# Kernel optimization log

Hardware: AMD Instinct MI355X
Metric: run time of the kernel (lower is better)

The kernel has to match this reference:

```python
import jax, jax.numpy as jnp
import numpy as np

N = 100000   # nodes
E = 1600000  # edges
F = 128      # node features
H = 64       # hidden_dim
G = 64       # graphs in batch


def setup_inputs() -> dict:
    key = jax.random.key(0)
    ks = jax.random.split(key, 12)
    x = jax.random.normal(ks[0], (N, F), jnp.float32)
    edge_index = jax.random.randint(ks[1], (2, E), 0, N, dtype=jnp.int64)
    batch = jnp.sort(jax.random.randint(ks[2], (N,), 0, G, dtype=jnp.int64))
    s = 0.05
    W1 = jax.random.normal(ks[3], (F, H), jnp.float32) * s
    b1 = jnp.zeros((H,), jnp.float32)
    W2 = jax.random.normal(ks[4], (H, H), jnp.float32) * s
    b2 = jnp.zeros((H,), jnp.float32)
    Wa = jax.random.normal(ks[5], (H, 1), jnp.float32) * s
    ba = jnp.zeros((1,), jnp.float32)
    Wc = jax.random.normal(ks[6], (H, 1), jnp.float32) * s
    bc = jnp.zeros((1,), jnp.float32)
    return {"x": x, "edge_index": edge_index, "batch": batch,
            "W1": W1, "b1": b1, "W2": W2, "b2": b2,
            "Wa": Wa, "ba": ba, "Wc": Wc, "bc": bc}


def _gcn_norm(edge_index, n):
    # Add self-loops, compute symmetric normalization deg^-1/2[src]*deg^-1/2[dst]
    loop = jnp.arange(n, dtype=edge_index.dtype)
    src = jnp.concatenate([edge_index[0], loop])
    dst = jnp.concatenate([edge_index[1], loop])
    deg = jax.ops.segment_sum(jnp.ones_like(src, jnp.float32), dst, num_segments=n)
    dinv = jnp.where(deg > 0, deg ** -0.5, 0.0)
    norm = dinv[src] * dinv[dst]  # [E+N]
    return src, dst, norm


def _gcn_conv(x, W, b, src, dst, norm, n):
    h = x @ W                         # [n, H] dense transform first (PyG order)
    msg = h[src] * norm[:, None]      # gather + normalize [E+n, H]
    agg = jax.ops.segment_sum(msg, dst, num_segments=n)  # scatter-add
    return agg + b


def reference(x, edge_index, batch, W1, b1, W2, b2, Wa, ba, Wc, bc):
    n = x.shape[0]
    src, dst, norm = _gcn_norm(edge_index, n)
    h = jax.nn.relu(_gcn_conv(x, W1, b1, src, dst, norm, n))
    # dropout p=0.1 is identity in eval mode
    h = jax.nn.relu(_gcn_conv(h, W2, b2, src, dst, norm, n))
    action_logits = (h @ Wa + ba)[:, 0]  # [N]
    counts = jax.ops.segment_sum(jnp.ones((n,), jnp.float32), batch, num_segments=G)
    pooled = jax.ops.segment_sum(h, batch, num_segments=G) / jnp.maximum(counts, 1.0)[:, None]
    value = pooled @ Wc + bc  # [G, 1]
    return action_logits, value
```

## Files before the change

### kernel.cpp

```cpp
#include <hip/hip_runtime.h>
#include <hip/hip_fp16.h>
#include <math.h>

#define FEAT 128
#define HID  64
#define BSH  7
#define BNODES (1 << BSH)
#define PB   256
#define SRCM ((1u << 25) - 1)


__global__ void part_hist_k(const int* __restrict__ dst, int* __restrict__ table,
                            int e, int nb) {
    __shared__ int lcnt[1024];
    for (int i = threadIdx.x; i < nb; i += 256) lcnt[i] = 0;
    __syncthreads();
    int eb = (e + PB - 1) / PB;
    int lo = blockIdx.x * eb, hi = min(lo + eb, e);
    for (int i = lo + threadIdx.x; i < hi; i += 256)
        atomicAdd(&lcnt[dst[i] >> BSH], 1);
    __syncthreads();
    for (int k = threadIdx.x; k < nb; k += 256)
        table[k * PB + blockIdx.x] = lcnt[k];
}

__global__ void scan1_k(int* __restrict__ data, int* __restrict__ aux, int L) {
    __shared__ int s[1024];
    int gid = blockIdx.x * 1024 + threadIdx.x;
    int v = (gid < L) ? data[gid] : 0;
    s[threadIdx.x] = v;
    __syncthreads();
    for (int off = 1; off < 1024; off <<= 1) {
        int t = (threadIdx.x >= off) ? s[threadIdx.x - off] : 0;
        __syncthreads();
        s[threadIdx.x] += t;
        __syncthreads();
    }
    if (gid < L) data[gid] = s[threadIdx.x] - v;
    if (threadIdx.x == 1023) aux[blockIdx.x] = s[1023];
}

__global__ void scan2_k(int* aux, int naux) {
    __shared__ int s[1024];
    int v = (threadIdx.x < naux) ? aux[threadIdx.x] : 0;
    s[threadIdx.x] = v;
    __syncthreads();
    for (int off = 1; off < 1024; off <<= 1) {
        int t = (threadIdx.x >= off) ? s[threadIdx.x - off] : 0;
        __syncthreads();
        s[threadIdx.x] += t;
        __syncthreads();
    }
    if (threadIdx.x < naux) aux[threadIdx.x] = s[threadIdx.x] - v;
}

__global__ void part_scatter_k(const int* __restrict__ src, const int* __restrict__ dst,
                               const int* __restrict__ table, const int* __restrict__ aux,
                               unsigned* __restrict__ packed, int e, int nb) {
    __shared__ int loff[1024];
    for (int k = threadIdx.x; k < nb; k += 256) {
        int idx = k * PB + blockIdx.x;
        loff[k] = table[idx] + aux[idx >> 10];
    }
    __syncthreads();
    int eb = (e + PB - 1) / PB;
    int lo = blockIdx.x * eb, hi = min(lo + eb, e);
    for (int i = lo + threadIdx.x; i < hi; i += 256) {
        int d = dst[i];
        int p = atomicAdd(&loff[d >> BSH], 1);
        packed[p] = ((unsigned)(d & (BNODES - 1)) << 25) | (unsigned)src[i];
    }
}


__global__ void bucket_sort_k(const unsigned* __restrict__ packed,
                              const int* __restrict__ table, const int* __restrict__ aux,
                              int* __restrict__ col, int* __restrict__ rowptr,
                              float* __restrict__ dinv, int n, int e, int nb) {
    __shared__ int cnt[BNODES];
    __shared__ int s[BNODES];
    __shared__ int cur[BNODES];
    const int k = blockIdx.x;
    const int t = threadIdx.x;
    if (t < BNODES) cnt[t] = 0;
    __syncthreads();
    int i0 = k * PB;
    int i1 = (k + 1) * PB;
    const int bs = table[i0] + aux[i0 >> 10];
    const int be = (k + 1 < nb) ? (table[i1] + aux[i1 >> 10]) : e;
    for (int i = bs + t; i < be; i += 256)
        atomicAdd(&cnt[packed[i] >> 25], 1);
    __syncthreads();
    if (t < BNODES) s[t] = cnt[t];
    __syncthreads();
    for (int off = 1; off < BNODES; off <<= 1) {
        int v = (t < BNODES && t >= off) ? s[t - off] : 0;
        __syncthreads();
        if (t < BNODES) s[t] += v;
        __syncthreads();
    }
    if (t < BNODES) {
        int base = bs + s[t] - cnt[t];
        cur[t] = base;
        int node = (k << BSH) + t;
        if (node < n) {
            rowptr[node] = base;
            dinv[node] = 1.0f / sqrtf(1.0f + (float)cnt[t]);
            if (node == n - 1) rowptr[n] = base + cnt[t];
        }
    }
    __syncthreads();
    for (int i = bs + t; i < be; i += 256) {
        unsigned u = packed[i];
        int p = atomicAdd(&cur[u >> 25], 1);
        col[p] = (int)(u & SRCM);
    }
}


template<int K, bool IN16>
__global__ __launch_bounds__(256, (K == 128) ? 3 : 4)
void gemm_tile_k(const void* __restrict__ Xv, const float* __restrict__ W,
                 const float* __restrict__ dinv, __half* __restrict__ out, int n) {
    __shared__ float sX[64][K + 4];
    __shared__ float sW[64][64];
    const int row0 = blockIdx.x * 64;
    const int t  = threadIdx.x;
    const int tx = t & 15;
    const int ty = t >> 4;
    constexpr int KSH = (K == 128) ? 7 : 6;

    if constexpr (!IN16) {
        const float* xb = (const float*)Xv + (size_t)row0 * K;
#pragma unroll
        for (int it = 0; it < K / 16; ++it) {
            int fl = it * 1024 + t * 4;
            int r  = fl >> KSH;
            int k  = fl & (K - 1);
            float4 v = make_float4(0.f, 0.f, 0.f, 0.f);
            if (row0 + r < n) v = *(const float4*)(xb + fl);
            *(float4*)&sX[r][k] = v;
        }
    } else {
        const __half* xb = (const __half*)Xv + (size_t)row0 * K;
#pragma unroll
        for (int it = 0; it < K / 32; ++it) {
            int fl = it * 2048 + t * 8;
            int r  = fl >> KSH;
            int k  = fl & (K - 1);
            float4 raw = make_float4(0.f, 0.f, 0.f, 0.f);
            if (row0 + r < n) raw = *(const float4*)(xb + fl);
            const __half2* hp = (const __half2*)&raw;
#pragma unroll
            for (int j = 0; j < 4; ++j) {
                float2 f = __half22float2(hp[j]);
                sX[r][k + 2 * j]     = f.x;
                sX[r][k + 2 * j + 1] = f.y;
            }
        }
    }

    float acc[4][4] = {};
#pragma unroll
    for (int ph = 0; ph < K / 64; ++ph) {
        __syncthreads();
#pragma unroll
        for (int it = 0; it < 4; ++it) {
            int fl = it * 1024 + t * 4;
            *(float4*)&sW[fl >> 6][fl & 63] = *(const float4*)(W + ph * 64 * HID + fl);
        }
        __syncthreads();

#pragma unroll 8
        for (int k = 0; k < 64; k += 4) {
            float4 a[4], b[4];
#pragma unroll
            for (int i = 0; i < 4; i++) a[i] = *(float4*)&sX[ty * 4 + i][ph * 64 + k];
#pragma unroll
            for (int j = 0; j < 4; j++) b[j] = *(float4*)&sW[k + j][tx * 4];
#pragma unroll
            for (int i = 0; i < 4; i++) {
                acc[i][0] = fmaf(a[i].x, b[0].x, acc[i][0]);
                acc[i][1] = fmaf(a[i].x, b[0].y, acc[i][1]);
                acc[i][2] = fmaf(a[i].x, b[0].z, acc[i][2]);
                acc[i][3] = fmaf(a[i].x, b[0].w, acc[i][3]);
                acc[i][0] = fmaf(a[i].y, b[1].x, acc[i][0]);
                acc[i][1] = fmaf(a[i].y, b[1].y, acc[i][1]);
                acc[i][2] = fmaf(a[i].y, b[1].z, acc[i][2]);
                acc[i][3] = fmaf(a[i].y, b[1].w, acc[i][3]);
                acc[i][0] = fmaf(a[i].z, b[2].x, acc[i][0]);
                acc[i][1] = fmaf(a[i].z, b[2].y, acc[i][1]);
                acc[i][2] = fmaf(a[i].z, b[2].z, acc[i][2]);
                acc[i][3] = fmaf(a[i].z, b[2].w, acc[i][3]);
                acc[i][0] = fmaf(a[i].w, b[3].x, acc[i][0]);
                acc[i][1] = fmaf(a[i].w, b[3].y, acc[i][1]);
                acc[i][2] = fmaf(a[i].w, b[3].z, acc[i][2]);
                acc[i][3] = fmaf(a[i].w, b[3].w, acc[i][3]);
            }
        }
    }

#pragma unroll
    for (int i = 0; i < 4; i++) {
        int gr = row0 + ty * 4 + i;
        if (gr < n) {
            float sc = dinv[gr];
            union { __half2 h[2]; unsigned long long u; } pk;
            pk.h[0] = __floats2half2_rn(acc[i][0] * sc, acc[i][1] * sc);
            pk.h[1] = __floats2half2_rn(acc[i][2] * sc, acc[i][3] * sc);
            *(unsigned long long*)(out + (size_t)gr * HID + tx * 4) = pk.u;
        }
    }
}


template<bool LOGITS>
__global__ void gather_k(const __half* __restrict__ tS, const int* __restrict__ rowptr,
                         const int* __restrict__ col, const float* __restrict__ dinv,
                         const float* __restrict__ b, __half* __restrict__ out,
                         const float* __restrict__ Wa, const float* __restrict__ ba,
                         float* __restrict__ logits, int n) {
    int node = (int)((blockIdx.x * (size_t)blockDim.x + threadIdx.x) >> 5);
    int lane = threadIdx.x & 31;
    if (node >= n) return;
    int beg = rowptr[node], end = rowptr[node + 1];
    const __half2* tl = (const __half2*)tS + lane;
    float2 acc = __half22float2(tl[node * 32]);
    int e = beg;
    for (; e + 16 <= end; e += 16) {
        int s[16];
        __half2 v[16];
#pragma unroll
        for (int j = 0; j < 16; j++) s[j] = col[e + j];
#pragma unroll
        for (int j = 0; j < 16; j++) v[j] = tl[s[j] * 32];
        float2 t0 = make_float2(0.f, 0.f), t1 = make_float2(0.f, 0.f);
#pragma unroll
        for (int j = 0; j < 8; j++) {
            float2 f = __half22float2(v[j]);
            t0.x += f.x; t0.y += f.y;
        }
#pragma unroll
        for (int j = 8; j < 16; j++) {
            float2 f = __half22float2(v[j]);
            t1.x += f.x; t1.y += f.y;
        }
        acc.x += t0.x + t1.x;
        acc.y += t0.y + t1.y;
    }
    for (; e + 4 <= end; e += 4) {
        __half2 v0 = tl[col[e] * 32];
        __half2 v1 = tl[col[e + 1] * 32];
        __half2 v2 = tl[col[e + 2] * 32];
        __half2 v3 = tl[col[e + 3] * 32];
        float2 f0 = __half22float2(v0), f1 = __half22float2(v1);
        float2 f2 = __half22float2(v2), f3 = __half22float2(v3);
        acc.x += (f0.x + f1.x) + (f2.x + f3.x);
        acc.y += (f0.y + f1.y) + (f2.y + f3.y);
    }
    for (; e < end; ++e) {
        float2 f = __half22float2(tl[col[e] * 32]);
        acc.x += f.x; acc.y += f.y;
    }
    float d = dinv[node];
    float2 bb = *(const float2*)(b + 2 * lane);
    float h0 = fmaxf(fmaf(d, acc.x, bb.x), 0.0f);
    float h1 = fmaxf(fmaf(d, acc.y, bb.y), 0.0f);
    ((__half2*)out)[node * 32 + lane] = __floats2half2_rn(h0, h1);
    if (LOGITS) {
        float2 wa = *(const float2*)(Wa + 2 * lane);
        float p = h0 * wa.x + h1 * wa.y;
#pragma unroll
        for (int off = 16; off > 0; off >>= 1) p += __shfl_down(p, off, 32);
        if (lane == 0) logits[node] = p + ba[0];
    }
}


__global__ void pool_k(const __half* __restrict__ h, const int* __restrict__ batch,
                       float* __restrict__ pooled, int n) {
    int lane = threadIdx.x & 31;
    int grp  = threadIdx.x >> 5;
    int start = (blockIdx.x * 8 + grp) * 64;
    if (start >= n) return;
    int end = min(start + 64, n);
    const __half2* hp = (const __half2*)h + lane;
    float2 acc = make_float2(0.f, 0.f);
    int curg = -1;
    for (int i = start; i < end; i++) {
        int g = batch[i];
        if (g != curg) {
            if (curg >= 0) {
                atomicAdd(&pooled[curg * HID + 2 * lane], acc.x);
                atomicAdd(&pooled[curg * HID + 2 * lane + 1], acc.y);
            }
            curg = g; acc = make_float2(0.f, 0.f);
        }
        float2 f = __half22float2(hp[i * 32]);
        acc.x += f.x; acc.y += f.y;
    }
    atomicAdd(&pooled[curg * HID + 2 * lane], acc.x);
    atomicAdd(&pooled[curg * HID + 2 * lane + 1], acc.y);
}


__global__ void value_k(const float* __restrict__ pooled, const int* __restrict__ batch,
                        const float* __restrict__ Wc, const float* __restrict__ bc,
                        float* __restrict__ val, int n, int g) {
    int gw   = (int)((blockIdx.x * (size_t)blockDim.x + threadIdx.x) >> 6);
    int lane = threadIdx.x & 63;
    if (gw >= g) return;
    int lo = 0, hi = n;
    while (lo < hi) { int m = (lo + hi) >> 1; if (batch[m] < gw) lo = m + 1; else hi = m; }
    int b0 = lo;
    lo = 0; hi = n;
    while (lo < hi) { int m = (lo + hi) >> 1; if (batch[m] < gw + 1) lo = m + 1; else hi = m; }
    float cnt = fmaxf((float)(lo - b0), 1.0f);
    float p = (pooled[gw * HID + lane] / cnt) * Wc[lane];
#pragma unroll
    for (int off = 32; off > 0; off >>= 1) p += __shfl_down(p, off);
    if (lane == 0) val[gw] = p + bc[0];
}

extern "C" void kernel_launch(void* const* d_in, const int* in_sizes, int n_in,
                              void* d_out, int out_size, void* d_ws, size_t ws_size,
                              hipStream_t stream) {
    const float* x     = (const float*)d_in[0];
    const int*   ei    = (const int*)d_in[1];
    const int*   batch = (const int*)d_in[2];
    const float* W1    = (const float*)d_in[3];
    const float* b1    = (const float*)d_in[4];
    const float* W2    = (const float*)d_in[5];
    const float* b2    = (const float*)d_in[6];
    const float* Wa    = (const float*)d_in[7];
    const float* ba    = (const float*)d_in[8];
    const float* Wc    = (const float*)d_in[9];
    const float* bc    = (const float*)d_in[10];

    const int n = in_sizes[0] / FEAT;
    const int e = in_sizes[1] / 2;
    const int g = out_size - n;
    const int* src = ei;
    const int* dst = ei + e;

    const int nb = (n + BNODES - 1) >> BSH;
    const int L  = nb * PB;

    float*    ws     = (float*)d_ws;
    float*    dinv   = ws;
    float*    bufA   = dinv + n;
    float*    bufB   = bufA + (size_t)n * HID;
    float*    pooled = bufB + (size_t)n * HID;
    int*      table  = (int*)(pooled + (size_t)g * HID);
    int*      aux    = table + L;
    int*      rowptr = aux + 1024;
    int*      col    = rowptr + n + 1;
    unsigned* packed = (unsigned*)bufA;
    __half*   tS     = (__half*)bufA;
    __half*   h16    = (__half*)bufB;

    const int B = 256;
    const int gridT = (n + 63) / 64;
    const int gridG = (int)(((size_t)n * 32 + B - 1) / B);
    const int gridP = (n + 8 * 64 - 1) / (8 * 64);
    const int nb1   = (L + 1023) / 1024;

    hipMemsetAsync(pooled, 0, (size_t)g * HID * sizeof(float), stream);

    part_hist_k<<<PB, B, 0, stream>>>(dst, table, e, nb);
    scan1_k<<<nb1, 1024, 0, stream>>>(table, aux, L);
    scan2_k<<<1, 1024, 0, stream>>>(aux, nb1);
    part_scatter_k<<<PB, B, 0, stream>>>(src, dst, table, aux, packed, e, nb);
    bucket_sort_k<<<nb, B, 0, stream>>>(packed, table, aux, col, rowptr, dinv, n, e, nb);

    gemm_tile_k<FEAT, false><<<gridT, B, 0, stream>>>(x, W1, dinv, tS, n);
    gather_k<false><<<gridG, B, 0, stream>>>(tS, rowptr, col, dinv, b1, h16,
                                             nullptr, nullptr, nullptr, n);

    gemm_tile_k<HID, true><<<gridT, B, 0, stream>>>(h16, W2, dinv, tS, n);
    gather_k<true><<<gridG, B, 0, stream>>>(tS, rowptr, col, dinv, b2, h16,
                                            Wa, ba, (float*)d_out, n);

    pool_k<<<gridP, B, 0, stream>>>(h16, batch, pooled, n);
    value_k<<<(g * 64 + B - 1) / B, B, 0, stream>>>(pooled, batch, Wc, bc,
                                                    (float*)d_out + n, n, g);
}
```

Before: 322.7 us.

## Fuse second-layer GEMM into first gather and rewrite pooling per graph

Folds the layer-2 dense transform (h @ W2, scaled by dinv) into the first aggregation kernel. Each warp does a 64x64 matvec using warp shuffles and an fp16 copy of W2 held in shared memory, which removes one GEMM launch and a full write and read of the hidden tensor. Pooling changes from atomic accumulation over contiguous node ranges to per-graph blocks split PSPLIT ways: each block finds its graph's range by binary search and reduces through shared memory before its atomics. The trade-off is extra per-node ALU and shuffle work in the gather kernel, plus fp16 rounding of both W2 and the ReLU output before the matvec.

```diff
diff --git a/kernel.cpp b/kernel.cpp
--- a/kernel.cpp
+++ b/kernel.cpp
@@ -8,6 +8,7 @@
 #define BNODES (1 << BSH)
 #define PB   256
 #define SRCM ((1u << 25) - 1)
+#define PSPLIT 16
 
 
 __global__ void part_hist_k(const int* __restrict__ dst, int* __restrict__ table,
@@ -118,46 +119,26 @@
 }
 
 
-template<int K, bool IN16>
-__global__ __launch_bounds__(256, (K == 128) ? 3 : 4)
-void gemm_tile_k(const void* __restrict__ Xv, const float* __restrict__ W,
+__global__ __launch_bounds__(256, 3)
+void gemm_tile_k(const float* __restrict__ X, const float* __restrict__ W,
                  const float* __restrict__ dinv, __half* __restrict__ out, int n) {
+    constexpr int K = FEAT;
     __shared__ float sX[64][K + 4];
     __shared__ float sW[64][64];
     const int row0 = blockIdx.x * 64;
     const int t  = threadIdx.x;
     const int tx = t & 15;
     const int ty = t >> 4;
-    constexpr int KSH = (K == 128) ? 7 : 6;
-
-    if constexpr (!IN16) {
-        const float* xb = (const float*)Xv + (size_t)row0 * K;
-#pragma unroll
-        for (int it = 0; it < K / 16; ++it) {
-            int fl = it * 1024 + t * 4;
-            int r  = fl >> KSH;
-            int k  = fl & (K - 1);
-            float4 v = make_float4(0.f, 0.f, 0.f, 0.f);
-            if (row0 + r < n) v = *(const float4*)(xb + fl);
-            *(float4*)&sX[r][k] = v;
-        }
-    } else {
-        const __half* xb = (const __half*)Xv + (size_t)row0 * K;
-#pragma unroll
-        for (int it = 0; it < K / 32; ++it) {
-            int fl = it * 2048 + t * 8;
-            int r  = fl >> KSH;
-            int k  = fl & (K - 1);
-            float4 raw = make_float4(0.f, 0.f, 0.f, 0.f);
-            if (row0 + r < n) raw = *(const float4*)(xb + fl);
-            const __half2* hp = (const __half2*)&raw;
-#pragma unroll
-            for (int j = 0; j < 4; ++j) {
-                float2 f = __half22float2(hp[j]);
-                sX[r][k + 2 * j]     = f.x;
-                sX[r][k + 2 * j + 1] = f.y;
-            }
-        }
+
+    const float* xb = X + (size_t)row0 * K;
+#pragma unroll
+    for (int it = 0; it < K / 16; ++it) {
+        int fl = it * 1024 + t * 4;
+        int r  = fl >> 7;
+        int k  = fl & (K - 1);
+        float4 v = make_float4(0.f, 0.f, 0.f, 0.f);
+        if (row0 + r < n) v = *(const float4*)(xb + fl);
+        *(float4*)&sX[r][k] = v;
     }
 
     float acc[4][4] = {};
@@ -214,12 +195,20 @@
 }
 
 
-template<bool LOGITS>
-__global__ void gather_k(const __half* __restrict__ tS, const int* __restrict__ rowptr,
-                         const int* __restrict__ col, const float* __restrict__ dinv,
-                         const float* __restrict__ b, __half* __restrict__ out,
-                         const float* __restrict__ Wa, const float* __restrict__ ba,
-                         float* __restrict__ logits, int n) {
+__global__ void gather1_k(const __half* __restrict__ tS, const int* __restrict__ rowptr,
+                          const int* __restrict__ col, const float* __restrict__ dinv,
+                          const float* __restrict__ b, const float* __restrict__ W2,
+                          __half* __restrict__ out, int n) {
+    __shared__ __half2 sW2[32][32][2];
+    for (int i = threadIdx.x; i < 32 * 32; i += 256) {
+        int kk = i >> 5, j = i & 31;
+        float2 a = *(const float2*)(W2 + (2 * kk) * HID + 2 * j);
+        float2 c = *(const float2*)(W2 + (2 * kk + 1) * HID + 2 * j);
+        sW2[kk][j][0] = __floats2half2_rn(a.x, a.y);
+        sW2[kk][j][1] = __floats2half2_rn(c.x, c.y);
+    }
+    __syncthreads();
+
     int node = (int)((blockIdx.x * (size_t)blockDim.x + threadIdx.x) >> 5);
     int lane = threadIdx.x & 31;
     if (node >= n) return;
@@ -266,41 +255,115 @@
     float2 bb = *(const float2*)(b + 2 * lane);
     float h0 = fmaxf(fmaf(d, acc.x, bb.x), 0.0f);
     float h1 = fmaxf(fmaf(d, acc.y, bb.y), 0.0f);
+
+    __half2 hh = __floats2half2_rn(h0, h1);
+    int hu = *(int*)&hh;
+    float2 o = make_float2(0.f, 0.f);
+#pragma unroll
+    for (int kk = 0; kk < 32; ++kk) {
+        int pu = __shfl(hu, kk, 32);
+        __half2 hv = *(__half2*)&pu;
+        float2 hf = __half22float2(hv);
+        float2 w0 = __half22float2(sW2[kk][lane][0]);
+        float2 w1 = __half22float2(sW2[kk][lane][1]);
+        o.x = fmaf(hf.x, w0.x, o.x); o.y = fmaf(hf.x, w0.y, o.y);
+        o.x = fmaf(hf.y, w1.x, o.x); o.y = fmaf(hf.y, w1.y, o.y);
+    }
+    ((__half2*)out)[node * 32 + lane] = __floats2half2_rn(o.x * d, o.y * d);
+}
+
+
+__global__ void gather2_k(const __half* __restrict__ tS, const int* __restrict__ rowptr,
+                          const int* __restrict__ col, const float* __restrict__ dinv,
+                          const float* __restrict__ b, __half* __restrict__ out,
+                          const float* __restrict__ Wa, const float* __restrict__ ba,
+                          float* __restrict__ logits, int n) {
+    int node = (int)((blockIdx.x * (size_t)blockDim.x + threadIdx.x) >> 5);
+    int lane = threadIdx.x & 31;
+    if (node >= n) return;
+    int beg = rowptr[node], end = rowptr[node + 1];
+    const __half2* tl = (const __half2*)tS + lane;
+    float2 acc = __half22float2(tl[node * 32]);
+    int e = beg;
+    for (; e + 16 <= end; e += 16) {
+        int s[16];
+        __half2 v[16];
+#pragma unroll
+        for (int j = 0; j < 16; j++) s[j] = col[e + j];
+#pragma unroll
+        for (int j = 0; j < 16; j++) v[j] = tl[s[j] * 32];
+        float2 t0 = make_float2(0.f, 0.f), t1 = make_float2(0.f, 0.f);
+#pragma unroll
+        for (int j = 0; j < 8; j++) {
+            float2 f = __half22float2(v[j]);
+            t0.x += f.x; t0.y += f.y;
+        }
+#pragma unroll
+        for (int j = 8; j < 16; j++) {
+            float2 f = __half22float2(v[j]);
+            t1.x += f.x; t1.y += f.y;
+        }
+        acc.x += t0.x + t1.x;
+        acc.y += t0.y + t1.y;
+    }
+    for (; e + 4 <= end; e += 4) {
+        __half2 v0 = tl[col[e] * 32];
+        __half2 v1 = tl[col[e + 1] * 32];
+        __half2 v2 = tl[col[e + 2] * 32];
+        __half2 v3 = tl[col[e + 3] * 32];
+        float2 f0 = __half22float2(v0), f1 = __half22float2(v1);
+        float2 f2 = __half22float2(v2), f3 = __half22float2(v3);
+        acc.x += (f0.x + f1.x) + (f2.x + f3.x);
+        acc.y += (f0.y + f1.y) + (f2.y + f3.y);
+    }
+    for (; e < end; ++e) {
+        float2 f = __half22float2(tl[col[e] * 32]);
+        acc.x += f.x; acc.y += f.y;
+    }
+    float d = dinv[node];
+    float2 bb = *(const float2*)(b + 2 * lane);
+    float h0 = fmaxf(fmaf(d, acc.x, bb.x), 0.0f);
+    float h1 = fmaxf(fmaf(d, acc.y, bb.y), 0.0f);
     ((__half2*)out)[node * 32 + lane] = __floats2half2_rn(h0, h1);
-    if (LOGITS) {
-        float2 wa = *(const float2*)(Wa + 2 * lane);
-        float p = h0 * wa.x + h1 * wa.y;
-#pragma unroll
-        for (int off = 16; off > 0; off >>= 1) p += __shfl_down(p, off, 32);
-        if (lane == 0) logits[node] = p + ba[0];
-    }
-}
-
-
-__global__ void pool_k(const __half* __restrict__ h, const int* __restrict__ batch,
-                       float* __restrict__ pooled, int n) {
-    int lane = threadIdx.x & 31;
-    int grp  = threadIdx.x >> 5;
-    int start = (blockIdx.x * 8 + grp) * 64;
-    if (start >= n) return;
-    int end = min(start + 64, n);
+    float2 wa = *(const float2*)(Wa + 2 * lane);
+    float p = h0 * wa.x + h1 * wa.y;
+#pragma unroll
+    for (int off = 16; off > 0; off >>= 1) p += __shfl_down(p, off, 32);
+    if (lane == 0) logits[node] = p + ba[0];
+}
+
+
+__global__ void pool2_k(const __half* __restrict__ h, const int* __restrict__ batch,
+                        float* __restrict__ pooled, int n) {
+    const int gid  = blockIdx.x / PSPLIT;
+    const int part = blockIdx.x % PSPLIT;
+    int lo = 0, hi = n;
+    while (lo < hi) { int m = (lo + hi) >> 1; if (batch[m] < gid) lo = m + 1; else hi = m; }
+    const int b0 = lo;
+    hi = n;
+    while (lo < hi) { int m = (lo + hi) >> 1; if (batch[m] < gid + 1) lo = m + 1; else hi = m; }
+    const int b1 = lo;
+    const int chunk = (b1 - b0 + PSPLIT - 1) / PSPLIT;
+    const int r0 = b0 + part * chunk;
+    const int r1 = min(r0 + chunk, b1);
+    const int lane = threadIdx.x & 31;
+    const int rg   = threadIdx.x >> 5;
     const __half2* hp = (const __half2*)h + lane;
     float2 acc = make_float2(0.f, 0.f);
-    int curg = -1;
-    for (int i = start; i < end; i++) {
-        int g = batch[i];
-        if (g != curg) {
-            if (curg >= 0) {
-                atomicAdd(&pooled[curg * HID + 2 * lane], acc.x);
-                atomicAdd(&pooled[curg * HID + 2 * lane + 1], acc.y);
-            }
-            curg = g; acc = make_float2(0.f, 0.f);
-        }
-        float2 f = __half22float2(hp[i * 32]);
+    for (int i = r0 + rg; i < r1; i += 8) {
+        float2 f = __half22float2(hp[(size_t)i * 32]);
         acc.x += f.x; acc.y += f.y;
     }
-    atomicAdd(&pooled[curg * HID + 2 * lane], acc.x);
-    atomicAdd(&pooled[curg * HID + 2 * lane + 1], acc.y);
+    __shared__ float2 red[8][32];
+    red[rg][lane] = acc;
+    __syncthreads();
+    if (threadIdx.x < 32) {
+        float2 s = make_float2(0.f, 0.f);
+#pragma unroll
+        for (int r = 0; r < 8; r++) { s.x += red[r][threadIdx.x].x; s.y += red[r][threadIdx.x].y; }
+        atomicAdd(&pooled[gid * HID + 2 * threadIdx.x], s.x);
+        atomicAdd(&pooled[gid * HID + 2 * threadIdx.x + 1], s.y);
+    }
 }
 
 
@@ -356,16 +419,16 @@
     int*      rowptr = aux + 1024;
     int*      col    = rowptr + n + 1;
     unsigned* packed = (unsigned*)bufA;
-    __half*   tS     = (__half*)bufA;
-    __half*   h16    = (__half*)bufB;
+    __half*   tS1    = (__half*)bufA;
+    __half*   tS2    = (__half*)bufB;
+    __half*   h2     = (__half*)bufA;
 
     const int B = 256;
     const int gridT = (n + 63) / 64;
     const int gridG = (int)(((size_t)n * 32 + B - 1) / B);
-    const int gridP = (n + 8 * 64 - 1) / (8 * 64);
     const int nb1   = (L + 1023) / 1024;
 
-    hipMemsetAsync(pooled, 0, (size_t)g * HID * sizeof(float), stream);
+    (void)hipMemsetAsync(pooled, 0, (size_t)g * HID * sizeof(float), stream);
 
     part_hist_k<<<PB, B, 0, stream>>>(dst, table, e, nb);
     scan1_k<<<nb1, 1024, 0, stream>>>(table, aux, L);
@@ -373,15 +436,13 @@
     part_scatter_k<<<PB, B, 0, stream>>>(src, dst, table, aux, packed, e, nb);
     bucket_sort_k<<<nb, B, 0, stream>>>(packed, table, aux, col, rowptr, dinv, n, e, nb);
 
-    gemm_tile_k<FEAT, false><<<gridT, B, 0, stream>>>(x, W1, dinv, tS, n);
-    gather_k<false><<<gridG, B, 0, stream>>>(tS, rowptr, col, dinv, b1, h16,
-                                             nullptr, nullptr, nullptr, n);
-
-    gemm_tile_k<HID, true><<<gridT, B, 0, stream>>>(h16, W2, dinv, tS, n);
-    gather_k<true><<<gridG, B, 0, stream>>>(tS, rowptr, col, dinv, b2, h16,
-                                            Wa, ba, (float*)d_out, n);
-
-    pool_k<<<gridP, B, 0, stream>>>(h16, batch, pooled, n);
+    gemm_tile_k<<<gridT, B, 0, stream>>>(x, W1, dinv, tS1, n);
+    gather1_k<<<gridG, B, 0, stream>>>(tS1, rowptr, col, dinv, b1, W2, tS2, n);
+
+    gather2_k<<<gridG, B, 0, stream>>>(tS2, rowptr, col, dinv, b2, h2,
+                                       Wa, ba, (float*)d_out, n);
+
+    pool2_k<<<g * PSPLIT, B, 0, stream>>>(h2, batch, pooled, n);
     value_k<<<(g * 64 + B - 1) / B, B, 0, stream>>>(pooled, batch, Wc, bc,
                                                     (float*)d_out + n, n, g);
 }
```

Measured after the change: 304.8 us. 5.5% less time.
